# Kernel tuning notes

Measured on AMD Instinct MI355X. Metric: run time of the kernel, lower is better.

The kernel has to match this reference:

```python
import jax, jax.numpy as jnp
import numpy as np

B, S, HID, NH, NS = 2, 1024, 2048, 16, 8
D = HID // NH  # head_dim = 128


def setup_inputs() -> dict:
    key = jax.random.key(0)
    ks = jax.random.split(key, 8)
    inv = 1.0 / np.sqrt(HID)
    return {
        "hidden_states": jax.random.normal(ks[0], (B, S, HID), jnp.float32),
        "Wq": jax.random.normal(ks[1], (HID, HID), jnp.float32) * inv,
        "Wk": jax.random.normal(ks[2], (HID, HID), jnp.float32) * inv,
        "Wv": jax.random.normal(ks[3], (HID, HID), jnp.float32) * inv,
        "Wo": jax.random.normal(ks[4], (HID, HID), jnp.float32) * inv,
        "splat_positions": jax.random.normal(ks[5], (NH, NS, D), jnp.float32) * 0.02,
        "splat_directions": jax.random.normal(ks[6], (NH, NS, D), jnp.float32) * 0.02,
        "splat_log_scales": jnp.full((NH, NS), np.log(0.8), jnp.float32),
        "splat_log_amplitudes": jnp.full((NH, NS), -np.log(float(NS)), jnp.float32),
        "directional_strength": jnp.float32(0.3),
        "gsa_strength": jnp.float32(-6.0),
    }


def _affinities(tokens, positions, directions, scales, dir_strength):
    # tokens [B,NH,S,D]; positions/directions [NH,NS,D]; scales [NH,NS]
    tok_sq = jnp.sum(tokens * tokens, axis=-1)                       # [B,NH,S]
    pos_sq = jnp.sum(positions * positions, axis=-1)                 # [NH,NS]
    tp = jnp.einsum('bhsd,hnd->bhsn', tokens, positions)             # [B,NH,S,NS]
    dist2 = tok_sq[..., None] - 2.0 * tp + pos_sq[None, :, None, :]
    dist2 = jnp.maximum(dist2, 0.0)
    # signed projection of (token - position) onto unit direction
    proj = (jnp.einsum('bhsd,hnd->bhsn', tokens, directions)
            - jnp.sum(positions * directions, axis=-1)[None, :, None, :])
    perp2 = jnp.maximum(dist2 - proj * proj, 0.0)
    inv2s2 = (0.5 / (scales * scales))[None, :, None, :]
    radial = jnp.exp(-dist2 * inv2s2)
    directional = jnp.exp(-perp2 * inv2s2)
    return (1.0 - dir_strength) * radial + dir_strength * directional


def reference(hidden_states, Wq, Wk, Wv, Wo, splat_positions, splat_directions,
              splat_log_scales, splat_log_amplitudes, directional_strength, gsa_strength):
    b, s, hid = hidden_states.shape

    def heads(x):  # [B,S,HID] -> [B,NH,S,D]
        return x.reshape(b, s, NH, D).transpose(0, 2, 1, 3)

    q = heads(hidden_states @ Wq)
    k = heads(hidden_states @ Wk)
    v = heads(hidden_states @ Wv)

    # --- standard (original) attention path ---
    scores = jnp.einsum('bhqd,bhkd->bhqk', q, k) / jnp.sqrt(jnp.float32(D))
    attn = jax.nn.softmax(scores, axis=-1)
    std = jnp.einsum('bhqk,bhkd->bhqd', attn, v)
    std = std.transpose(0, 2, 1, 3).reshape(b, s, hid) @ Wo

    # --- directional GSA path ---
    eps = 1e-12
    positions = splat_positions / (jnp.linalg.norm(splat_positions, axis=-1, keepdims=True) + eps)
    positions = positions * (np.sqrt(D) * 0.3)
    directions = splat_directions / (jnp.linalg.norm(splat_directions, axis=-1, keepdims=True) + eps)
    scales = jnp.clip(jnp.exp(splat_log_scales), 0.3, 1.2)
    amplitudes = jax.nn.softmax(splat_log_amplitudes, axis=-1)
    ds = jax.nn.sigmoid(directional_strength)

    qa = _affinities(q, positions, directions, scales, ds)  # [B,NH,S,NS]
    ka = _affinities(k, positions, directions, scales, ds)  # [B,NH,S,NS]
    w = jnp.einsum('bhqn,hn,bhkn->bhqk', qa, amplitudes, ka)
    w = w / (jnp.sum(w, axis=-1, keepdims=True) + 1e-8)
    dgsa = jnp.einsum('bhqk,bhkd->bhqd', w, v)
    dgsa = dgsa.transpose(0, 2, 1, 3).reshape(b, s, hid) @ Wo

    gsa = jax.nn.sigmoid(gsa_strength)
    blend = jnp.minimum(0.05, gsa * 0.1)
    return (1.0 - blend) * std + blend * dgsa
```

## Files before the change

### kernel.cpp

```cpp
#include <hip/hip_runtime.h>
#include <math.h>

typedef __attribute__((ext_vector_type(8))) short bf16x8;
typedef __attribute__((ext_vector_type(4))) float f32x4;
typedef unsigned short ushort_t;

#define SQRT_D 11.313708498984761f
#define INV_SQRT_D 0.08838834764831845f

__device__ __forceinline__ unsigned short f2b(float f) {
    unsigned u = __float_as_uint(f);
    unsigned r = (u + 0x7fffu + ((u >> 16) & 1u)) >> 16;
    return (unsigned short)r;
}
__device__ __forceinline__ float b2f(unsigned short h) {
    return __uint_as_float(((unsigned)h) << 16);
}

__device__ __forceinline__ void async_copy16(const void* g, void* l) {
    __builtin_amdgcn_global_load_lds((const __attribute__((address_space(1))) void*)g,
                                     (__attribute__((address_space(3))) void*)l, 16, 0, 0);
}

__global__ __launch_bounds__(256) void prep(
    const float* __restrict__ X, const float* __restrict__ W0,
    const float* __restrict__ W1, const float* __restrict__ W2,
    const float* __restrict__ W3, const float* __restrict__ sp,
    const float* __restrict__ sd, const float* __restrict__ ls,
    const float* __restrict__ la, ushort_t* __restrict__ Xbf,
    ushort_t* __restrict__ WT4, float* __restrict__ posn,
    float* __restrict__ dirn, float* __restrict__ pos_sq,
    float* __restrict__ pdv, float* __restrict__ iv2s2,
    float* __restrict__ amp) {
    __shared__ float t[64][65];
    const int z = blockIdx.z;
    const int tid = threadIdx.x;
    if (z < 4) {
        const float* W = (z == 0) ? W0 : (z == 1) ? W1 : (z == 2) ? W2 : W3;
        ushort_t* WT = WT4 + (size_t)z * 4194304;
        const int bn = blockIdx.x * 64, bk = blockIdx.y * 64;
        const int c4 = (tid & 15) * 4;
        const int r0 = tid >> 4;
#pragma unroll
        for (int p = 0; p < 4; ++p) {
            int r = r0 + p * 16;
            float4 v = *(const float4*)(W + (size_t)(bk + r) * 2048 + bn + c4);
            t[r][c4] = v.x; t[r][c4 + 1] = v.y; t[r][c4 + 2] = v.z; t[r][c4 + 3] = v.w;
        }
        __syncthreads();
#pragma unroll
        for (int p = 0; p < 4; ++p) {
            int n = r0 + p * 16;
            ushort4 o;
            o.x = f2b(t[c4][n]);     o.y = f2b(t[c4 + 1][n]);
            o.z = f2b(t[c4 + 2][n]); o.w = f2b(t[c4 + 3][n]);
            *(ushort4*)(WT + (size_t)(bn + n) * 2048 + bk + c4) = o;
        }
        return;
    }
    {
        int bi = blockIdx.y * 32 + blockIdx.x;
#pragma unroll
        for (int p = 0; p < 4; ++p) {
            int i = (((bi * 4 + p) * 256) + tid) * 4;
            float4 v = *(const float4*)(X + i);
            ushort4 o;
            o.x = f2b(v.x); o.y = f2b(v.y); o.z = f2b(v.z); o.w = f2b(v.w);
            *(ushort4*)(Xbf + i) = o;
        }
    }
    if (blockIdx.x == 0 && blockIdx.y == 0 && tid < 128) {
        int i = tid;
        const float* p = sp + (size_t)i * 128;
        const float* d = sd + (size_t)i * 128;
        float np_ = 0.f, nd_ = 0.f;
        for (int k = 0; k < 128; ++k) { np_ += p[k] * p[k]; nd_ += d[k] * d[k]; }
        np_ = sqrtf(np_); nd_ = sqrtf(nd_);
        const float sc = 3.394112549695428f;
        float rp = sc / (np_ + 1e-12f);
        float rd = 1.f / (nd_ + 1e-12f);
        float psq = 0.f, pd_ = 0.f;
        for (int k = 0; k < 128; ++k) {
            float pn = p[k] * rp;
            float dn = d[k] * rd;
            posn[(size_t)i * 128 + k] = pn;
            dirn[(size_t)i * 128 + k] = dn;
            psq += pn * pn;
            pd_ += pn * dn;
        }
        pos_sq[i] = psq;
        pdv[i] = pd_;
        float s = expf(ls[i]);
        s = fminf(fmaxf(s, 0.3f), 1.2f);
        iv2s2[i] = 0.5f / (s * s);
        if ((i & 7) == 0) {
            int h = i >> 3;
            float mx = -INFINITY;
            for (int n = 0; n < 8; ++n) mx = fmaxf(mx, la[h * 8 + n]);
            float e[8]; float ssum = 0.f;
            for (int n = 0; n < 8; ++n) { e[n] = expf(la[h * 8 + n] - mx); ssum += e[n]; }
            for (int n = 0; n < 8; ++n) amp[h * 8 + n] = e[n] / ssum;
        }
    }
}


__global__ __launch_bounds__(256) void gemm_qkv(const ushort_t* __restrict__ A,
                                                const ushort_t* __restrict__ WT4,
                                                ushort_t* __restrict__ Qb,
                                                ushort_t* __restrict__ Kb,
                                                ushort_t* __restrict__ Vb,
                                                ushort_t* __restrict__ Vt) {
    __shared__ ushort_t As0[128 * 32], As1[128 * 32];
    __shared__ ushort_t Bs0[128 * 32], Bs1[128 * 32];
    const int tid = threadIdx.x, lane = tid & 63, wave = tid >> 6;
    const int l15 = lane & 15, quad = lane >> 4;
    const int wm = (wave >> 1) * 64, wn = (wave & 1) * 64;
    const int bm = blockIdx.x * 128;
    const int by = blockIdx.y, which = by >> 4, bn = (by & 15) * 128;
    const ushort_t* BT = WT4 + (size_t)which * 4194304;
    f32x4 acc[4][4] = {};
    const int off0 = tid * 16;
    const int row0 = tid >> 2;
    const int c0 = (tid & 3) ^ ((row0 + (row0 >> 2)) & 3);
    const ushort_t* ga = A + (size_t)(bm + row0) * 2048 + c0 * 8;
    const ushort_t* gb = BT + (size_t)(bn + row0) * 2048 + c0 * 8;
    const int rsw = (l15 + (l15 >> 2)) & 3;
#define STAGEG(ABUF, BBUF, k_)                                                 \
    {                                                                          \
        async_copy16(ga + (k_), (char*)(ABUF) + off0);                         \
        async_copy16(ga + (size_t)64 * 2048 + (k_), (char*)(ABUF) + off0 + 4096); \
        async_copy16(gb + (k_), (char*)(BBUF) + off0);                         \
        async_copy16(gb + (size_t)64 * 2048 + (k_), (char*)(BBUF) + off0 + 4096); \
    }
#define COMPUTEG(ABUF, BBUF)                                                   \
    {                                                                          \
        bf16x8 af[4], bfr[4];                                                  \
        _Pragma("unroll") for (int i = 0; i < 4; ++i)                          \
            af[i] = *(const bf16x8*)((const char*)(ABUF) + (wm + i * 16 + l15) * 64 + ((quad ^ rsw) << 4)); \
        _Pragma("unroll") for (int j = 0; j < 4; ++j)                          \
            bfr[j] = *(const bf16x8*)((const char*)(BBUF) + (wn + j * 16 + l15) * 64 + ((quad ^ rsw) << 4)); \
        _Pragma("unroll") for (int i = 0; i < 4; ++i)                          \
            _Pragma("unroll") for (int j = 0; j < 4; ++j)                      \
                acc[i][j] = __builtin_amdgcn_mfma_f32_16x16x32_bf16(af[i], bfr[j], acc[i][j], 0, 0, 0); \
    }
    STAGEG(As0, Bs0, 0);
    for (int k0 = 0; k0 < 2048; k0 += 64) {
        __syncthreads();
        STAGEG(As1, Bs1, k0 + 32);
        COMPUTEG(As0, Bs0);
        __syncthreads();
        if (k0 + 64 < 2048) STAGEG(As0, Bs0, k0 + 64);
        COMPUTEG(As1, Bs1);
    }
#undef STAGEG
#undef COMPUTEG
    ushort_t* Cb = (which == 0) ? Qb : ((which == 1) ? Kb : Vb);
    const bool dot = (which == 2);
    const float oscale = (which == 0) ? INV_SQRT_D : 1.f;
#pragma unroll
    for (int i = 0; i < 4; ++i) {
#pragma unroll
        for (int j = 0; j < 4; ++j) {
            int m0 = bm + wm + i * 16 + quad * 4;
            int n = bn + wn + j * 16 + l15;
            int b = m0 >> 10, s0 = m0 & 1023, h = n >> 7, d = n & 127;
            ushort4 pack;
            unsigned short* pp = (unsigned short*)&pack;
#pragma unroll
            for (int r = 0; r < 4; ++r) {
                unsigned short bv = f2b(acc[i][j][r] * oscale);
                pp[r] = bv;
                Cb[((size_t)((b << 4) | h) * 1024 + (s0 + r)) * 128 + d] = bv;
            }
            if (dot) *(ushort4*)(Vt + ((size_t)((b << 4) | h) * 128 + d) * 1024 + s0) = pack;
        }
    }
}

__global__ __launch_bounds__(256) void gemm_out(const ushort_t* __restrict__ A,
                                                const ushort_t* __restrict__ BT,
                                                float* __restrict__ Cf) {
    __shared__ ushort_t As0[128 * 32], As1[128 * 32];
    __shared__ ushort_t Bs0[128 * 32], Bs1[128 * 32];
    const int tid = threadIdx.x, lane = tid & 63, wave = tid >> 6;
    const int l15 = lane & 15, quad = lane >> 4;
    const int wm = (wave >> 1) * 64, wn = (wave & 1) * 64;
    const int bm = blockIdx.x * 128, bn = blockIdx.y * 128;
    f32x4 acc[4][4] = {};
    const int off0 = tid * 16;
    const int row0 = tid >> 2;
    const int c0 = (tid & 3) ^ ((row0 + (row0 >> 2)) & 3);
    const ushort_t* ga = A + (size_t)(bm + row0) * 2048 + c0 * 8;
    const ushort_t* gb = BT + (size_t)(bn + row0) * 2048 + c0 * 8;
    const int rsw = (l15 + (l15 >> 2)) & 3;
#define STAGEO(ABUF, BBUF, k_)                                                 \
    {                                                                          \
        async_copy16(ga + (k_), (char*)(ABUF) + off0);                         \
        async_copy16(ga + (size_t)64 * 2048 + (k_), (char*)(ABUF) + off0 + 4096); \
        async_copy16(gb + (k_), (char*)(BBUF) + off0);                         \
        async_copy16(gb + (size_t)64 * 2048 + (k_), (char*)(BBUF) + off0 + 4096); \
    }
#define COMPUTEO(ABUF, BBUF)                                                   \
    {                                                                          \
        bf16x8 af[4], bfr[4];                                                  \
        _Pragma("unroll") for (int i = 0; i < 4; ++i)                          \
            af[i] = *(const bf16x8*)((const char*)(ABUF) + (wm + i * 16 + l15) * 64 + ((quad ^ rsw) << 4)); \
        _Pragma("unroll") for (int j = 0; j < 4; ++j)                          \
            bfr[j] = *(const bf16x8*)((const char*)(BBUF) + (wn + j * 16 + l15) * 64 + ((quad ^ rsw) << 4)); \
        _Pragma("unroll") for (int i = 0; i < 4; ++i)                          \
            _Pragma("unroll") for (int j = 0; j < 4; ++j)                      \
                acc[i][j] = __builtin_amdgcn_mfma_f32_16x16x32_bf16(af[i], bfr[j], acc[i][j], 0, 0, 0); \
    }
    STAGEO(As0, Bs0, 0);
    for (int k0 = 0; k0 < 2048; k0 += 64) {
        __syncthreads();
        STAGEO(As1, Bs1, k0 + 32);
        COMPUTEO(As0, Bs0);
        __syncthreads();
        if (k0 + 64 < 2048) STAGEO(As0, Bs0, k0 + 64);
        COMPUTEO(As1, Bs1);
    }
#undef STAGEO
#undef COMPUTEO
#pragma unroll
    for (int i = 0; i < 4; ++i)
#pragma unroll
        for (int j = 0; j < 4; ++j)
#pragma unroll
            for (int r = 0; r < 4; ++r) {
                int m = bm + wm + i * 16 + quad * 4 + r;
                int n = bn + wn + j * 16 + l15;
                Cf[(size_t)m * 2048 + n] = acc[i][j][r];
            }
}

__global__ __launch_bounds__(256) void affinity_q(
    const ushort_t* __restrict__ Q,
    const float* __restrict__ posn, const float* __restrict__ dirn,
    const float* __restrict__ pos_sq, const float* __restrict__ pdv,
    const float* __restrict__ iv2s2, const float* __restrict__ ds_in,
    float* __restrict__ qa) {
    int gid = blockIdx.x * 256 + threadIdx.x;
    int n = gid & 7;
    int t = gid >> 3;
    const ushort_t* T = Q + (size_t)t * 128;
    int h = (t >> 10) & 15;
    const float* P = posn + (size_t)(h * 8 + n) * 128;
    const float* Dr = dirn + (size_t)(h * 8 + n) * 128;
    float tsq = 0.f, tp = 0.f, td = 0.f;
#pragma unroll
    for (int d = 0; d < 128; d += 8) {
        uint4 raw = *(const uint4*)(T + d);
        float tv[8];
        tv[0] = __uint_as_float(raw.x << 16); tv[1] = __uint_as_float(raw.x & 0xffff0000u);
        tv[2] = __uint_as_float(raw.y << 16); tv[3] = __uint_as_float(raw.y & 0xffff0000u);
        tv[4] = __uint_as_float(raw.z << 16); tv[5] = __uint_as_float(raw.z & 0xffff0000u);
        tv[6] = __uint_as_float(raw.w << 16); tv[7] = __uint_as_float(raw.w & 0xffff0000u);
        float4 p0 = *(const float4*)(P + d), p1 = *(const float4*)(P + d + 4);
        float4 d0 = *(const float4*)(Dr + d), d1 = *(const float4*)(Dr + d + 4);
        tsq += tv[0]*tv[0]+tv[1]*tv[1]+tv[2]*tv[2]+tv[3]*tv[3]+tv[4]*tv[4]+tv[5]*tv[5]+tv[6]*tv[6]+tv[7]*tv[7];
        tp  += tv[0]*p0.x+tv[1]*p0.y+tv[2]*p0.z+tv[3]*p0.w+tv[4]*p1.x+tv[5]*p1.y+tv[6]*p1.z+tv[7]*p1.w;
        td  += tv[0]*d0.x+tv[1]*d0.y+tv[2]*d0.z+tv[3]*d0.w+tv[4]*d1.x+tv[5]*d1.y+tv[6]*d1.z+tv[7]*d1.w;
    }
    const float fs = SQRT_D;
    tsq *= fs * fs; tp *= fs; td *= fs;
    float dist2 = fmaxf(tsq - 2.f * tp + pos_sq[h * 8 + n], 0.f);
    float proj = td - pdv[h * 8 + n];
    float perp2 = fmaxf(dist2 - proj * proj, 0.f);
    float iv = iv2s2[h * 8 + n];
    float dsv = 1.f / (1.f + __expf(-ds_in[0]));
    float aff = (1.f - dsv) * __expf(-dist2 * iv) + dsv * __expf(-perp2 * iv);
    qa[(size_t)t * 8 + n] = aff;
}

__global__ __launch_bounds__(128) void kv_s1_part(
    const ushort_t* __restrict__ K, const ushort_t* __restrict__ V,
    const float* __restrict__ posn, const float* __restrict__ dirn,
    const float* __restrict__ pos_sq, const float* __restrict__ pdv,
    const float* __restrict__ iv2s2, const float* __restrict__ ds_in,
    float* __restrict__ KVp, float* __restrict__ S1p) {
    __shared__ float kas[64][8];
    int bh = blockIdx.x, sc = blockIdx.y;
    int tid = threadIdx.x;
    int h = bh & 15;
    if (tid < 64) {
        const ushort_t* T = K + ((size_t)bh * 1024 + sc * 64 + tid) * 128;
        float tsq = 0.f, tp[8] = {}, td[8] = {};
        for (int d = 0; d < 128; d += 4) {
            uint2 raw = *(const uint2*)(T + d);
            float t0 = __uint_as_float(raw.x << 16), t1 = __uint_as_float(raw.x & 0xffff0000u);
            float t2 = __uint_as_float(raw.y << 16), t3 = __uint_as_float(raw.y & 0xffff0000u);
            tsq += t0 * t0 + t1 * t1 + t2 * t2 + t3 * t3;
#pragma unroll
            for (int n = 0; n < 8; ++n) {
                const float* P = posn + (size_t)(h * 8 + n) * 128 + d;
                const float* Dr = dirn + (size_t)(h * 8 + n) * 128 + d;
                tp[n] += t0 * P[0] + t1 * P[1] + t2 * P[2] + t3 * P[3];
                td[n] += t0 * Dr[0] + t1 * Dr[1] + t2 * Dr[2] + t3 * Dr[3];
            }
        }
        float dsv = 1.f / (1.f + __expf(-ds_in[0]));
#pragma unroll
        for (int n = 0; n < 8; ++n) {
            float dist2 = fmaxf(tsq - 2.f * tp[n] + pos_sq[h * 8 + n], 0.f);
            float proj = td[n] - pdv[h * 8 + n];
            float perp2 = fmaxf(dist2 - proj * proj, 0.f);
            float iv = iv2s2[h * 8 + n];
            kas[tid][n] = (1.f - dsv) * __expf(-dist2 * iv) + dsv * __expf(-perp2 * iv);
        }
    }
    __syncthreads();
    int d = tid;
    const ushort_t* VB = V + ((size_t)bh * 1024 + sc * 64) * 128;
    float acc[8] = {};
#pragma unroll 4
    for (int s = 0; s < 64; ++s) {
        float vd = b2f(VB[(size_t)s * 128 + d]);
#pragma unroll
        for (int n = 0; n < 8; ++n) acc[n] += kas[s][n] * vd;
    }
#pragma unroll
    for (int n = 0; n < 8; ++n) KVp[(((size_t)bh * 8 + n) * 16 + sc) * 128 + d] = acc[n];
    __shared__ float s1p[128];
    {
        int n = d >> 4, chunk = d & 15;
        float p = 0.f;
        for (int s = chunk * 4; s < chunk * 4 + 4; ++s) p += kas[s][n];
        s1p[d] = p;
    }
    __syncthreads();
    if (d < 8) {
        float t = 0.f;
        for (int c = 0; c < 16; ++c) t += s1p[(d << 4) + c];
        S1p[((size_t)bh * 8 + d) * 16 + sc] = t;
    }
}

__global__ __launch_bounds__(256) void flash_blend(
    const ushort_t* __restrict__ Qg, const ushort_t* __restrict__ Kg,
    const ushort_t* __restrict__ Vtg,
    const float* __restrict__ qa, const float* __restrict__ amp,
    const float* __restrict__ S1p, const float* __restrict__ KVp,
    const float* __restrict__ gstr, ushort_t* __restrict__ blended) {
    __shared__ ushort_t Ks0[64 * 128], Ks1[64 * 128];
    __shared__ ushort_t Vt0[128 * 64], Vt1[128 * 64];
    __shared__ ushort_t Ps[4][16 * 72];
    __shared__ float KVs[8 * 128];
    __shared__ float S1s[8];
    const int tid = threadIdx.x, lane = tid & 63, wave = tid >> 6;
    const int l15 = lane & 15, quad = lane >> 4;
    const int bh = blockIdx.y, qt = blockIdx.x;

    const ushort_t* Qrow = Qg + ((size_t)(bh * 1024 + qt * 64 + wave * 16 + l15)) * 128 + quad * 8;
    bf16x8 aq[4];
#pragma unroll
    for (int k4 = 0; k4 < 4; ++k4) aq[k4] = *(const bf16x8*)(Qrow + k4 * 32);

    {
        int n = tid >> 5, d = (tid & 31) * 4;
        f32x4 kv = {};
#pragma unroll
        for (int sc = 0; sc < 16; ++sc)
            kv += *(const f32x4*)(KVp + (((size_t)bh * 8 + n) * 16 + sc) * 128 + d);
        *(f32x4*)(KVs + tid * 4) = kv;
    }
    if (tid < 8) {
        float s = 0.f;
#pragma unroll
        for (int sc = 0; sc < 16; ++sc) s += S1p[((size_t)bh * 8 + tid) * 16 + sc];
        S1s[tid] = s;
    }

    const ushort_t* Kbase = Kg + (size_t)bh * 131072;
    const ushort_t* Vbase = Vtg + (size_t)bh * 131072;

#define STAGE(KBUF, VBUF, kt_)                                                        \
    {                                                                                 \
        _Pragma("unroll") for (int i_ = 0; i_ < 4; ++i_) {                            \
            int off_ = tid * 16 + i_ * 4096;                                          \
            int kr_ = off_ >> 8, kp_ = (off_ >> 4) & 15;                              \
            async_copy16(Kbase + (size_t)(kt_)*8192 + kr_ * 128 + ((kp_ ^ (kr_ & 15)) << 3), \
                         (char*)(KBUF) + off_);                                       \
            int vd_ = off_ >> 7, vp_ = (off_ >> 4) & 7;                               \
            async_copy16(Vbase + (size_t)vd_ * 1024 + (kt_)*64 + ((vp_ ^ (vd_ & 7)) << 3), \
                         (char*)(VBUF) + off_);                                       \
        }                                                                             \
    }
#define FLASH_STEP(KBUF, VBUF)                                                        \
    {                                                                                 \
        f32x4 sc[4] = {};                                                             \
        _Pragma("unroll") for (int k4 = 0; k4 < 4; ++k4) {                            \
            _Pragma("unroll") for (int t = 0; t < 4; ++t) {                           \
                bf16x8 bk = *(const bf16x8*)((const char*)(KBUF) +                    \
                                             ((t * 16 + l15) << 8) + (((k4 * 4 + quad) ^ l15) << 4)); \
                sc[t] = __builtin_amdgcn_mfma_f32_16x16x32_bf16(aq[k4], bk, sc[t], 0, 0, 0); \
            }                                                                         \
        }                                                                             \
        _Pragma("unroll") for (int t = 0; t < 4; ++t) {                               \
            _Pragma("unroll") for (int r = 0; r < 4; ++r) {                           \
                float p = __expf(sc[t][r]);                                           \
                l_i[r] += p;                                                          \
                Pw[(quad * 4 + r) * 72 + t * 16 + l15] = f2b(p);                      \
            }                                                                         \
        }                                                                             \
        bf16x8 ap0 = *(const bf16x8*)((const char*)Pw + (l15 * 72 + quad * 8) * 2);   \
        bf16x8 ap1 = *(const bf16x8*)((const char*)Pw + (l15 * 72 + 32 + quad * 8) * 2); \
        _Pragma("unroll") for (int j = 0; j < 8; ++j) {                               \
            bf16x8 bv0 = *(const bf16x8*)((const char*)(VBUF) +                       \
                                          ((j * 16 + l15) << 7) + (((quad) ^ (l15 & 7)) << 4)); \
            bf16x8 bv1 = *(const bf16x8*)((const char*)(VBUF) +                       \
                                          ((j * 16 + l15) << 7) + (((4 + quad) ^ (l15 & 7)) << 4)); \
            o[j] = __builtin_amdgcn_mfma_f32_16x16x32_bf16(ap0, bv0, o[j], 0, 0, 0);  \
            o[j] = __builtin_amdgcn_mfma_f32_16x16x32_bf16(ap1, bv1, o[j], 0, 0, 0);  \
        }                                                                             \
    }

    STAGE(Ks0, Vt0, 0);

    f32x4 o[8] = {};
    float l_i[4] = {};
    ushort_t* Pw = &Ps[wave][0];

    for (int kt = 0; kt < 16; kt += 2) {
        __syncthreads();
        STAGE(Ks1, Vt1, kt + 1);
        FLASH_STEP(Ks0, Vt0);
        __syncthreads();
        if (kt + 2 < 16) STAGE(Ks0, Vt0, kt + 2);
        FLASH_STEP(Ks1, Vt1);
    }
#undef STAGE
#undef FLASH_STEP
#pragma unroll
    for (int r = 0; r < 4; ++r) {
        float l = l_i[r];
        l += __shfl_xor(l, 1);
        l += __shfl_xor(l, 2);
        l += __shfl_xor(l, 4);
        l += __shfl_xor(l, 8);
        l_i[r] = l;
    }
    float gsa = 1.f / (1.f + __expf(-gstr[0]));
    float blend = fminf(0.05f, gsa * 0.1f);
    int b = bh >> 4, h = bh & 15;
#pragma unroll
    for (int r = 0; r < 4; ++r) {
        int q = qt * 64 + wave * 16 + quad * 4 + r;
        const float* qaRow = qa + ((size_t)bh * 1024 + q) * 8;
        float qam[8], Z = 0.f;
#pragma unroll
        for (int n = 0; n < 8; ++n) {
            qam[n] = qaRow[n] * amp[h * 8 + n];
            Z += qam[n] * S1s[n];
        }
        float invZ = 1.f / (Z + 1e-8f);
        float invl = 1.f / l_i[r];
        ushort_t* outp = blended + ((size_t)(b * 1024 + q)) * 2048 + h * 128;
#pragma unroll
        for (int j = 0; j < 8; ++j) {
            int d = j * 16 + l15;
            float dg = 0.f;
#pragma unroll
            for (int n = 0; n < 8; ++n) dg += qam[n] * KVs[n * 128 + d];
            float v = (1.f - blend) * (o[j][r] * invl) + blend * (dg * invZ);
            outp[d] = f2b(v);
        }
    }
}

extern "C" void kernel_launch(void* const* d_in, const int* in_sizes, int n_in,
                              void* d_out, int out_size, void* d_ws, size_t ws_size,
                              hipStream_t stream) {
    const float* X = (const float*)d_in[0];
    const float* Wq = (const float*)d_in[1];
    const float* Wk = (const float*)d_in[2];
    const float* Wv = (const float*)d_in[3];
    const float* Wo = (const float*)d_in[4];
    const float* sp = (const float*)d_in[5];
    const float* sd = (const float*)d_in[6];
    const float* ls = (const float*)d_in[7];
    const float* la = (const float*)d_in[8];
    const float* dstr = (const float*)d_in[9];
    const float* gstr = (const float*)d_in[10];

    char* base = (char*)d_ws;
    ushort_t* WT4 = (ushort_t*)base;      base += 33554432;
    ushort_t* Xbf = (ushort_t*)base;      base += 8388608;
    ushort_t* blended = Xbf;
    ushort_t* Qbf = (ushort_t*)base;      base += 8388608;
    ushort_t* Kbf = (ushort_t*)base;      base += 8388608;
    ushort_t* Vbf = (ushort_t*)base;      base += 8388608;
    ushort_t* Vtb = (ushort_t*)base;      base += 8388608;
    float* qaw = (float*)base;            base += 1048576;
    float* posn = (float*)base;           base += 65536;
    float* dirn = (float*)base;           base += 65536;
    float* pos_sq = (float*)base;         base += 512;
    float* pdv = (float*)base;            base += 512;
    float* iv2s2 = (float*)base;          base += 512;
    float* ampw = (float*)base;           base += 512;
    float* S1p = (float*)base;            base += 16384;
    float* KVp = (float*)base;            base += 2097152;

    prep<<<dim3(32, 32, 5), 256, 0, stream>>>(X, Wq, Wk, Wv, Wo, sp, sd, ls, la,
                                              Xbf, WT4, posn, dirn, pos_sq, pdv, iv2s2, ampw);
    gemm_qkv<<<dim3(16, 48), 256, 0, stream>>>(Xbf, WT4, Qbf, Kbf, Vbf, Vtb);
    affinity_q<<<1024, 256, 0, stream>>>(Qbf, posn, dirn, pos_sq, pdv, iv2s2, dstr, qaw);
    kv_s1_part<<<dim3(32, 16), 128, 0, stream>>>(Kbf, Vbf, posn, dirn, pos_sq, pdv, iv2s2,
                                                 dstr, KVp, S1p);
    flash_blend<<<dim3(16, 32), 256, 0, stream>>>(Qbf, Kbf, Vtb, qaw, ampw, S1p, KVp,
                                                  gstr, blended);
    gemm_out<<<dim3(16, 16), 256, 0, stream>>>(blended, WT4 + 12582912, (float*)d_out);
}
```

Baseline: 325.1 us.

## Fuse query affinity computation into flash kernel and parallelize KV affinity reduction

Removes the standalone affinity_q launch and computes query-splat affinities inside flash_blend from the Q fragments already held in registers, reducing them across lanes with shuffles and keeping them in shared memory. This drops a kernel launch plus the round trip of the qa buffer. kv_s1_part now uses all 128 threads for the K affinity dot products, with a shared-memory partial reduction. The KV accumulation uses vectorized 8-wide V loads and folds the S1 row sums into the same loop. The cost is extra register pressure and prologue work in the flash kernel, which could lower its occupancy.

Result: no change. 321.7 us (median of 2 runs) (-1.0%).

```diff
diff --git a/kernel.cpp b/kernel.cpp
--- a/kernel.cpp
+++ b/kernel.cpp
@@ -235,112 +235,89 @@
             }
 }
 
-__global__ __launch_bounds__(256) void affinity_q(
-    const ushort_t* __restrict__ Q,
-    const float* __restrict__ posn, const float* __restrict__ dirn,
-    const float* __restrict__ pos_sq, const float* __restrict__ pdv,
-    const float* __restrict__ iv2s2, const float* __restrict__ ds_in,
-    float* __restrict__ qa) {
-    int gid = blockIdx.x * 256 + threadIdx.x;
-    int n = gid & 7;
-    int t = gid >> 3;
-    const ushort_t* T = Q + (size_t)t * 128;
-    int h = (t >> 10) & 15;
-    const float* P = posn + (size_t)(h * 8 + n) * 128;
-    const float* Dr = dirn + (size_t)(h * 8 + n) * 128;
-    float tsq = 0.f, tp = 0.f, td = 0.f;
-#pragma unroll
-    for (int d = 0; d < 128; d += 8) {
-        uint4 raw = *(const uint4*)(T + d);
-        float tv[8];
-        tv[0] = __uint_as_float(raw.x << 16); tv[1] = __uint_as_float(raw.x & 0xffff0000u);
-        tv[2] = __uint_as_float(raw.y << 16); tv[3] = __uint_as_float(raw.y & 0xffff0000u);
-        tv[4] = __uint_as_float(raw.z << 16); tv[5] = __uint_as_float(raw.z & 0xffff0000u);
-        tv[6] = __uint_as_float(raw.w << 16); tv[7] = __uint_as_float(raw.w & 0xffff0000u);
-        float4 p0 = *(const float4*)(P + d), p1 = *(const float4*)(P + d + 4);
-        float4 d0 = *(const float4*)(Dr + d), d1 = *(const float4*)(Dr + d + 4);
-        tsq += tv[0]*tv[0]+tv[1]*tv[1]+tv[2]*tv[2]+tv[3]*tv[3]+tv[4]*tv[4]+tv[5]*tv[5]+tv[6]*tv[6]+tv[7]*tv[7];
-        tp  += tv[0]*p0.x+tv[1]*p0.y+tv[2]*p0.z+tv[3]*p0.w+tv[4]*p1.x+tv[5]*p1.y+tv[6]*p1.z+tv[7]*p1.w;
-        td  += tv[0]*d0.x+tv[1]*d0.y+tv[2]*d0.z+tv[3]*d0.w+tv[4]*d1.x+tv[5]*d1.y+tv[6]*d1.z+tv[7]*d1.w;
-    }
-    const float fs = SQRT_D;
-    tsq *= fs * fs; tp *= fs; td *= fs;
-    float dist2 = fmaxf(tsq - 2.f * tp + pos_sq[h * 8 + n], 0.f);
-    float proj = td - pdv[h * 8 + n];
-    float perp2 = fmaxf(dist2 - proj * proj, 0.f);
-    float iv = iv2s2[h * 8 + n];
-    float dsv = 1.f / (1.f + __expf(-ds_in[0]));
-    float aff = (1.f - dsv) * __expf(-dist2 * iv) + dsv * __expf(-perp2 * iv);
-    qa[(size_t)t * 8 + n] = aff;
-}
-
 __global__ __launch_bounds__(128) void kv_s1_part(
     const ushort_t* __restrict__ K, const ushort_t* __restrict__ V,
     const float* __restrict__ posn, const float* __restrict__ dirn,
     const float* __restrict__ pos_sq, const float* __restrict__ pdv,
     const float* __restrict__ iv2s2, const float* __restrict__ ds_in,
     float* __restrict__ KVp, float* __restrict__ S1p) {
+    __shared__ float parts[128][17];
     __shared__ float kas[64][8];
-    int bh = blockIdx.x, sc = blockIdx.y;
-    int tid = threadIdx.x;
-    int h = bh & 15;
-    if (tid < 64) {
-        const ushort_t* T = K + ((size_t)bh * 1024 + sc * 64 + tid) * 128;
+    const int bh = blockIdx.x, sc = blockIdx.y;
+    const int tid = threadIdx.x;
+    const int h = bh & 15;
+    {
+        const int tk = tid & 63, half = tid >> 6;
+        const ushort_t* T = K + ((size_t)bh * 1024 + sc * 64 + tk) * 128 + half * 64;
+        const float* Pb = posn + (size_t)(h * 8) * 128 + half * 64;
+        const float* Db = dirn + (size_t)(h * 8) * 128 + half * 64;
         float tsq = 0.f, tp[8] = {}, td[8] = {};
-        for (int d = 0; d < 128; d += 4) {
+        for (int d = 0; d < 64; d += 4) {
             uint2 raw = *(const uint2*)(T + d);
             float t0 = __uint_as_float(raw.x << 16), t1 = __uint_as_float(raw.x & 0xffff0000u);
             float t2 = __uint_as_float(raw.y << 16), t3 = __uint_as_float(raw.y & 0xffff0000u);
             tsq += t0 * t0 + t1 * t1 + t2 * t2 + t3 * t3;
 #pragma unroll
             for (int n = 0; n < 8; ++n) {
-                const float* P = posn + (size_t)(h * 8 + n) * 128 + d;
-                const float* Dr = dirn + (size_t)(h * 8 + n) * 128 + d;
-                tp[n] += t0 * P[0] + t1 * P[1] + t2 * P[2] + t3 * P[3];
-                td[n] += t0 * Dr[0] + t1 * Dr[1] + t2 * Dr[2] + t3 * Dr[3];
+                float4 p = *(const float4*)(Pb + (size_t)n * 128 + d);
+                float4 e = *(const float4*)(Db + (size_t)n * 128 + d);
+                tp[n] += t0 * p.x + t1 * p.y + t2 * p.z + t3 * p.w;
+                td[n] += t0 * e.x + t1 * e.y + t2 * e.z + t3 * e.w;
             }
         }
+        parts[tid][0] = tsq;
+#pragma unroll
+        for (int n = 0; n < 8; ++n) { parts[tid][1 + n] = tp[n]; parts[tid][9 + n] = td[n]; }
+    }
+    __syncthreads();
+    if (tid < 64) {
         float dsv = 1.f / (1.f + __expf(-ds_in[0]));
+        float tsq = parts[tid][0] + parts[tid + 64][0];
 #pragma unroll
         for (int n = 0; n < 8; ++n) {
-            float dist2 = fmaxf(tsq - 2.f * tp[n] + pos_sq[h * 8 + n], 0.f);
-            float proj = td[n] - pdv[h * 8 + n];
+            float tp = parts[tid][1 + n] + parts[tid + 64][1 + n];
+            float td = parts[tid][9 + n] + parts[tid + 64][9 + n];
+            float dist2 = fmaxf(tsq - 2.f * tp + pos_sq[h * 8 + n], 0.f);
+            float proj = td - pdv[h * 8 + n];
             float perp2 = fmaxf(dist2 - proj * proj, 0.f);
             float iv = iv2s2[h * 8 + n];
             kas[tid][n] = (1.f - dsv) * __expf(-dist2 * iv) + dsv * __expf(-perp2 * iv);
         }
     }
     __syncthreads();
-    int d = tid;
-    const ushort_t* VB = V + ((size_t)bh * 1024 + sc * 64) * 128;
-    float acc[8] = {};
+    {
+        const int n = tid >> 4, d8 = tid & 15;
+        const ushort_t* VB = V + ((size_t)bh * 1024 + sc * 64) * 128 + d8 * 8;
+        f32x4 a0 = {}, a1 = {};
+        float s1 = 0.f;
 #pragma unroll 4
-    for (int s = 0; s < 64; ++s) {
-        float vd = b2f(VB[(size_t)s * 128 + d]);
-#pragma unroll
-        for (int n = 0; n < 8; ++n) acc[n] += kas[s][n] * vd;
-    }
-#pragma unroll
-    for (int n = 0; n < 8; ++n) KVp[(((size_t)bh * 8 + n) * 16 + sc) * 128 + d] = acc[n];
-    __shared__ float s1p[128];
-    {
-        int n = d >> 4, chunk = d & 15;
-        float p = 0.f;
-        for (int s = chunk * 4; s < chunk * 4 + 4; ++s) p += kas[s][n];
-        s1p[d] = p;
-    }
-    __syncthreads();
-    if (d < 8) {
-        float t = 0.f;
-        for (int c = 0; c < 16; ++c) t += s1p[(d << 4) + c];
-        S1p[((size_t)bh * 8 + d) * 16 + sc] = t;
+        for (int s = 0; s < 64; ++s) {
+            bf16x8 v8 = *(const bf16x8*)(VB + (size_t)s * 128);
+            float ka = kas[s][n];
+            s1 += ka;
+            a0[0] += ka * b2f((unsigned short)v8[0]);
+            a0[1] += ka * b2f((unsigned short)v8[1]);
+            a0[2] += ka * b2f((unsigned short)v8[2]);
+            a0[3] += ka * b2f((unsigned short)v8[3]);
+            a1[0] += ka * b2f((unsigned short)v8[4]);
+            a1[1] += ka * b2f((unsigned short)v8[5]);
+            a1[2] += ka * b2f((unsigned short)v8[6]);
+            a1[3] += ka * b2f((unsigned short)v8[7]);
+        }
+        float* outp = KVp + (((size_t)bh * 8 + n) * 16 + sc) * 128 + d8 * 8;
+        *(f32x4*)outp = a0;
+        *(f32x4*)(outp + 4) = a1;
+        if (d8 == 0) S1p[((size_t)bh * 8 + n) * 16 + sc] = s1;
     }
 }
 
 __global__ __launch_bounds__(256) void flash_blend(
     const ushort_t* __restrict__ Qg, const ushort_t* __restrict__ Kg,
     const ushort_t* __restrict__ Vtg,
-    const float* __restrict__ qa, const float* __restrict__ amp,
+    const float* __restrict__ posn, const float* __restrict__ dirn,
+    const float* __restrict__ pos_sq, const float* __restrict__ pdv,
+    const float* __restrict__ iv2s2, const float* __restrict__ dstr,
+    const float* __restrict__ amp,
     const float* __restrict__ S1p, const float* __restrict__ KVp,
     const float* __restrict__ gstr, ushort_t* __restrict__ blended) {
     __shared__ ushort_t Ks0[64 * 128], Ks1[64 * 128];
@@ -348,14 +325,60 @@
     __shared__ ushort_t Ps[4][16 * 72];
     __shared__ float KVs[8 * 128];
     __shared__ float S1s[8];
+    __shared__ float qas[4][16][8];
     const int tid = threadIdx.x, lane = tid & 63, wave = tid >> 6;
     const int l15 = lane & 15, quad = lane >> 4;
     const int bh = blockIdx.y, qt = blockIdx.x;
+    const int h = bh & 15;
 
     const ushort_t* Qrow = Qg + ((size_t)(bh * 1024 + qt * 64 + wave * 16 + l15)) * 128 + quad * 8;
     bf16x8 aq[4];
 #pragma unroll
     for (int k4 = 0; k4 < 4; ++k4) aq[k4] = *(const bf16x8*)(Qrow + k4 * 32);
+
+    {
+        const float dsv = 1.f / (1.f + __expf(-dstr[0]));
+        float tsq = 0.f, tp[8] = {}, td[8] = {};
+#pragma unroll
+        for (int k4 = 0; k4 < 4; ++k4) {
+            float tv[8];
+#pragma unroll
+            for (int j = 0; j < 8; ++j) tv[j] = b2f((unsigned short)aq[k4][j]);
+            const int d0 = k4 * 32 + quad * 8;
+#pragma unroll
+            for (int j = 0; j < 8; ++j) tsq += tv[j] * tv[j];
+#pragma unroll
+            for (int n = 0; n < 8; ++n) {
+                const float* P = posn + (size_t)(h * 8 + n) * 128 + d0;
+                const float* Dr = dirn + (size_t)(h * 8 + n) * 128 + d0;
+                float4 p0 = *(const float4*)P, p1 = *(const float4*)(P + 4);
+                float4 e0 = *(const float4*)Dr, e1 = *(const float4*)(Dr + 4);
+                tp[n] += tv[0] * p0.x + tv[1] * p0.y + tv[2] * p0.z + tv[3] * p0.w
+                       + tv[4] * p1.x + tv[5] * p1.y + tv[6] * p1.z + tv[7] * p1.w;
+                td[n] += tv[0] * e0.x + tv[1] * e0.y + tv[2] * e0.z + tv[3] * e0.w
+                       + tv[4] * e1.x + tv[5] * e1.y + tv[6] * e1.z + tv[7] * e1.w;
+            }
+        }
+        tsq += __shfl_xor(tsq, 16); tsq += __shfl_xor(tsq, 32);
+#pragma unroll
+        for (int n = 0; n < 8; ++n) {
+            tp[n] += __shfl_xor(tp[n], 16); tp[n] += __shfl_xor(tp[n], 32);
+            td[n] += __shfl_xor(td[n], 16); td[n] += __shfl_xor(td[n], 32);
+        }
+        if (quad == 0) {
+            const float fs = SQRT_D;
+            float ts = tsq * fs * fs;
+#pragma unroll
+            for (int n = 0; n < 8; ++n) {
+                float tpn = tp[n] * fs, tdn = td[n] * fs;
+                float dist2 = fmaxf(ts - 2.f * tpn + pos_sq[h * 8 + n], 0.f);
+                float proj = tdn - pdv[h * 8 + n];
+                float perp2 = fmaxf(dist2 - proj * proj, 0.f);
+                float iv = iv2s2[h * 8 + n];
+                qas[wave][l15][n] = (1.f - dsv) * __expf(-dist2 * iv) + dsv * __expf(-perp2 * iv);
+            }
+        }
+    }
 
     {
         int n = tid >> 5, d = (tid & 31) * 4;
@@ -443,11 +466,11 @@
     }
     float gsa = 1.f / (1.f + __expf(-gstr[0]));
     float blend = fminf(0.05f, gsa * 0.1f);
-    int b = bh >> 4, h = bh & 15;
+    int b = bh >> 4;
 #pragma unroll
     for (int r = 0; r < 4; ++r) {
         int q = qt * 64 + wave * 16 + quad * 4 + r;
-        const float* qaRow = qa + ((size_t)bh * 1024 + q) * 8;
+        const float* qaRow = &qas[wave][quad * 4 + r][0];
         float qam[8], Z = 0.f;
 #pragma unroll
         for (int n = 0; n < 8; ++n) {
@@ -492,7 +515,6 @@
     ushort_t* Kbf = (ushort_t*)base;      base += 8388608;
     ushort_t* Vbf = (ushort_t*)base;      base += 8388608;
     ushort_t* Vtb = (ushort_t*)base;      base += 8388608;
-    float* qaw = (float*)base;            base += 1048576;
     float* posn = (float*)base;           base += 65536;
     float* dirn = (float*)base;           base += 65536;
     float* pos_sq = (float*)base;         base += 512;
@@ -505,10 +527,9 @@
     prep<<<dim3(32, 32, 5), 256, 0, stream>>>(X, Wq, Wk, Wv, Wo, sp, sd, ls, la,
                                               Xbf, WT4, posn, dirn, pos_sq, pdv, iv2s2, ampw);
     gemm_qkv<<<dim3(16, 48), 256, 0, stream>>>(Xbf, WT4, Qbf, Kbf, Vbf, Vtb);
-    affinity_q<<<1024, 256, 0, stream>>>(Qbf, posn, dirn, pos_sq, pdv, iv2s2, dstr, qaw);
     kv_s1_part<<<dim3(32, 16), 128, 0, stream>>>(Kbf, Vbf, posn, dirn, pos_sq, pdv, iv2s2,
                                                  dstr, KVp, S1p);
-    flash_blend<<<dim3(16, 32), 256, 0, stream>>>(Qbf, Kbf, Vtb, qaw, ampw, S1p, KVp,
-                                                  gstr, blended);
+    flash_blend<<<dim3(16, 32), 256, 0, stream>>>(Qbf, Kbf, Vtb, posn, dirn, pos_sq, pdv,
+                                                  iv2s2, dstr, ampw, S1p, KVp, gstr, blended);
     gemm_out<<<dim3(16, 16), 256, 0, stream>>>(blended, WT4 + 12582912, (float*)d_out);
 }
```
